# Optimization experiments

Hardware: AMD Instinct MI355X
Metric: run time of the kernel (lower is better)

Reference implementation:

```python
import jax, jax.numpy as jnp
import numpy as np

SEQ_LEN = 70      # hardcoded in original (view(-1, 70))
HIDDEN = 230
EMB = 50
VOCAB = 100000
BIG_NUM = 64
N_TOTAL = 2048
N_REL = 100       # hardcoded relation count
POS_VOCAB = 123
POS_DIM = 5
D_IN = EMB + 2 * POS_DIM


def setup_inputs() -> dict:
    key = jax.random.key(0)
    ks = jax.random.split(key, 20)
    bag = N_TOTAL // BIG_NUM
    labels = jax.random.randint(ks[3], (BIG_NUM,), 0, N_REL)
    inp = {
        "sentence": jax.random.randint(ks[0], (N_TOTAL, SEQ_LEN), 0, VOCAB),
        "pos1": jax.random.randint(ks[1], (N_TOTAL, SEQ_LEN), 0, POS_VOCAB),
        "pos2": jax.random.randint(ks[2], (N_TOTAL, SEQ_LEN), 0, POS_VOCAB),
        "total_shape": jnp.arange(BIG_NUM + 1, dtype=jnp.int32) * bag,
        "y_batch": jax.nn.one_hot(labels, N_REL, dtype=jnp.float32),
        "word_emb": jax.random.normal(ks[4], (VOCAB, EMB), jnp.float32) * 0.1,
        "pos1_table": jax.random.normal(ks[5], (POS_VOCAB, POS_DIM), jnp.float32) * 0.1,
        "pos2_table": jax.random.normal(ks[6], (POS_VOCAB, POS_DIM), jnp.float32) * 0.1,
        "W_ih_f": jax.random.normal(ks[7], (3 * HIDDEN, D_IN), jnp.float32) * 0.05,
        "W_hh_f": jax.random.normal(ks[8], (3 * HIDDEN, HIDDEN), jnp.float32) * 0.05,
        "b_ih_f": jnp.zeros((3 * HIDDEN,), jnp.float32),
        "b_hh_f": jnp.zeros((3 * HIDDEN,), jnp.float32),
        "W_ih_b": jax.random.normal(ks[9], (3 * HIDDEN, D_IN), jnp.float32) * 0.05,
        "W_hh_b": jax.random.normal(ks[10], (3 * HIDDEN, HIDDEN), jnp.float32) * 0.05,
        "b_ih_b": jnp.zeros((3 * HIDDEN,), jnp.float32),
        "b_hh_b": jnp.zeros((3 * HIDDEN,), jnp.float32),
        "attention_w": jax.random.normal(ks[11], (HIDDEN, 1), jnp.float32) * 0.1,
        "sen_a": jax.random.normal(ks[12], (HIDDEN,), jnp.float32) * 0.1,
        "sen_r": jax.random.normal(ks[13], (HIDDEN, 1), jnp.float32) * 0.1,
        "relation_embedding": jax.random.normal(ks[14], (N_REL, HIDDEN), jnp.float32) * 0.1,
        "sen_d": jax.random.normal(ks[15], (N_REL,), jnp.float32) * 0.1,
    }
    return inp


def _gru_dir(x_proj, W_hh, b_hh, reverse):
    """One GRU direction. x_proj: [N,T,3H] = x @ W_ih^T + b_ih (precomputed)."""
    N = x_proj.shape[0]
    H = W_hh.shape[1]

    def step(h, gi):
        gh = h @ W_hh.T + b_hh
        i_r, i_z, i_n = jnp.split(gi, 3, axis=-1)
        h_r, h_z, h_n = jnp.split(gh, 3, axis=-1)
        r = jax.nn.sigmoid(i_r + h_r)
        z = jax.nn.sigmoid(i_z + h_z)
        n = jnp.tanh(i_n + r * h_n)
        h = (1.0 - z) * n + z * h
        return h, h

    h0 = jnp.zeros((N, H), x_proj.dtype)
    _, ys = jax.lax.scan(step, h0, jnp.swapaxes(x_proj, 0, 1), reverse=reverse)
    return jnp.swapaxes(ys, 0, 1)  # [N,T,H]


def reference(sentence, pos1, pos2, total_shape, y_batch,
              word_emb, pos1_table, pos2_table,
              W_ih_f, W_hh_f, b_ih_f, b_hh_f,
              W_ih_b, W_hh_b, b_ih_b, b_hh_b,
              attention_w, sen_a, sen_r, relation_embedding, sen_d):
    # embedding lookup + concat -> [N, T, D_IN]
    emb = jnp.concatenate([word_emb[sentence], pos1_table[pos1], pos2_table[pos2]], axis=-1)
    gi_f = jnp.einsum('ntd,gd->ntg', emb, W_ih_f) + b_ih_f
    gi_b = jnp.einsum('ntd,gd->ntg', emb, W_ih_b) + b_ih_b
    # bidirectional GRU, then sum fwd + bwd halves (torch.add(tupf, tupb))
    tup = _gru_dir(gi_f, W_hh_f, b_hh_f, False) + _gru_dir(gi_b, W_hh_b, b_hh_b, True)  # [N,T,H]
    # word-level attention over the 70 timesteps
    word_alpha = jax.nn.softmax((jnp.tanh(tup) @ attention_w)[..., 0], axis=-1)  # [N,T]
    attention_r = jnp.einsum('nt,nth->nh', word_alpha, tup)                       # [N,H]
    repre = jnp.tanh(attention_r)
    # ragged per-bag (sentence-level) attention via segment ops
    n_total = repre.shape[0]
    seg = jnp.searchsorted(total_shape[1:], jnp.arange(n_total), side='right')   # [N] bag ids
    s = ((repre * sen_a) @ sen_r)[:, 0]                                          # [N]
    m = jax.ops.segment_max(s, seg, num_segments=BIG_NUM)
    e = jnp.exp(s - m[seg])
    denom = jax.ops.segment_sum(e, seg, num_segments=BIG_NUM)
    alpha = e / denom[seg]
    sen_s = jax.ops.segment_sum(alpha[:, None] * repre, seg, num_segments=BIG_NUM)  # [B,H]
    logits = sen_s @ relation_embedding.T + sen_d                                   # [B,100]
    prob = jax.nn.softmax(logits, axis=-1)
    # BCEWithLogitsLoss (mean over 100 classes) summed over bags
    bce = jnp.maximum(logits, 0.0) - logits * y_batch + jnp.log1p(jnp.exp(-jnp.abs(logits)))
    total_loss = jnp.sum(jnp.mean(bce, axis=-1))
    acc = (jnp.argmax(prob, axis=-1) == jnp.argmax(y_batch, axis=-1)).astype(jnp.float32)
    return total_loss, acc, prob
```

## Files before the change

### kernel.cpp

```cpp
#include <hip/hip_runtime.h>
#include <hip/hip_bf16.h>
#include <math.h>

#define SEQ 70
#define HID 230
#define G3  690
#define EMBD 50
#define DIN 60
#define NTOT 2048
#define NREL 100
#define NBAG 64
#define BAGSZ 32
#define PDIM 5
#define MB 8
#define KU 10
#define KTOT 290
#define SROWS 292


__global__ void k_zero(float* p, long n) {
    long i = (long)blockIdx.x * 256 + threadIdx.x;
    if (i < n) p[i] = 0.f;
}

__global__ void k_embed(const int* __restrict__ sent, const int* __restrict__ p1,
                        const int* __restrict__ p2,  const float* __restrict__ wemb,
                        const float* __restrict__ t1, const float* __restrict__ t2,
                        float* __restrict__ emb) {
    long idx = (long)blockIdx.x * 256 + threadIdx.x;
    long total = (long)NTOT * SEQ * DIN;
    if (idx >= total) return;
    int nt = (int)(idx / DIN);
    int j  = (int)(idx % DIN);
    float v;
    if (j < EMBD)            v = wemb[(long)sent[nt] * EMBD + j];
    else if (j < EMBD + PDIM) v = t1[p1[nt] * PDIM + (j - EMBD)];
    else                      v = t2[p2[nt] * PDIM + (j - EMBD - PDIM)];
    emb[idx] = v;
}

__global__ void k_transpose(const float* __restrict__ in, float* __restrict__ out,
                            int G, int K) {
    int idx = blockIdx.x * 256 + threadIdx.x;
    if (idx >= G * K) return;
    int g = idx / K, k = idx % K;
    out[k * G + g] = in[idx];
}


#define ROWLD(R0,R1, kk) { const float4* _p = (const float4*)s_s[kk]; \
    R0 = _p[0]; R1 = _p[1]; }

#define FMA4(WR,WZ,WN, Q, B, AR,AZ,AN) \
    AR[B+0]=fmaf(WR,Q.x,AR[B+0]); AZ[B+0]=fmaf(WZ,Q.x,AZ[B+0]); AN[B+0]=fmaf(WN,Q.x,AN[B+0]); \
    AR[B+1]=fmaf(WR,Q.y,AR[B+1]); AZ[B+1]=fmaf(WZ,Q.y,AZ[B+1]); AN[B+1]=fmaf(WN,Q.y,AN[B+1]); \
    AR[B+2]=fmaf(WR,Q.z,AR[B+2]); AZ[B+2]=fmaf(WZ,Q.z,AZ[B+2]); AN[B+2]=fmaf(WN,Q.z,AN[B+2]); \
    AR[B+3]=fmaf(WR,Q.w,AR[B+3]); AZ[B+3]=fmaf(WZ,Q.w,AZ[B+3]); AN[B+3]=fmaf(WN,Q.w,AN[B+3]);

#define FMA8(WR,WZ,WN, AR,AZ,AN, Q0,Q1) \
    FMA4(WR,WZ,WN, Q0, 0, AR,AZ,AN) FMA4(WR,WZ,WN, Q1, 4, AR,AZ,AN)

#define U2R(KB, UE, AR,AZ,AN) \
    FMA8(wR[UE],wZ[UE],wN[UE], AR,AZ,AN, ra0,ra1); \
    ROWLD(ra0,ra1, (KB)*KU+(UE)+2); \
    { int _kk = (((KB)+1)*KU + (UE)) * G3; wR[UE]=pr[_kk]; wZ[UE]=pz[_kk]; wN[UE]=pn[_kk]; } \
    FMA8(wR[UE+1],wZ[UE+1],wN[UE+1], AR,AZ,AN, rb0,rb1); \
    ROWLD(rb0,rb1, (KB)*KU+(UE)+3); \
    { int _kk = (((KB)+1)*KU + (UE)+1) * G3; wR[UE+1]=pr[_kk]; wZ[UE+1]=pz[_kk]; wN[UE+1]=pn[_kk]; }

#define U2W(KB, UE, AR,AZ,AN) \
    FMA8(wR[UE],wZ[UE],wN[UE], AR,AZ,AN, ra0,ra1); \
    ROWLD(ra0,ra1, (KB)*KU+(UE)+2); \
    { int _kk = (UE) * G3; wR[UE]=pr[_kk]; wZ[UE]=pz[_kk]; wN[UE]=pn[_kk]; } \
    FMA8(wR[UE+1],wZ[UE+1],wN[UE+1], AR,AZ,AN, rb0,rb1); \
    ROWLD(rb0,rb1, (KB)*KU+(UE)+3); \
    { int _kk = ((UE)+1) * G3; wR[UE+1]=pr[_kk]; wZ[UE+1]=pz[_kk]; wN[UE+1]=pn[_kk]; }

#define BLK10R(KB, AR,AZ,AN) \
    U2R(KB, 0, AR,AZ,AN) U2R(KB, 2, AR,AZ,AN) U2R(KB, 4, AR,AZ,AN) \
    U2R(KB, 6, AR,AZ,AN) U2R(KB, 8, AR,AZ,AN)

#define BLK10W(KB, AR,AZ,AN) \
    U2W(KB, 0, AR,AZ,AN) U2W(KB, 2, AR,AZ,AN) U2W(KB, 4, AR,AZ,AN) \
    U2W(KB, 6, AR,AZ,AN) U2W(KB, 8, AR,AZ,AN)

__global__ __launch_bounds__(256, 2) void k_gru(
    const float* __restrict__ emb,
    const float* __restrict__ wcat_f, const float* __restrict__ bih_f, const float* __restrict__ bhh_f,
    const float* __restrict__ wcat_b, const float* __restrict__ bih_b, const float* __restrict__ bhh_b,
    float* __restrict__ tup) {

    const bool rev = blockIdx.x & 1;
    const int  n0  = (blockIdx.x >> 1) * MB;
    const float* wcat = rev ? wcat_b : wcat_f;
    const float* bih  = rev ? bih_b  : bih_f;
    const float* bhh  = rev ? bhh_b  : bhh_f;
    const int tid = threadIdx.x;
    const bool act = tid < HID;

    __shared__ float s_s[SROWS][MB];

    for (int i = tid; i < SROWS * MB; i += 256) ((float*)s_s)[i] = 0.f;

    float bir = 0.f, biz = 0.f, bin_ = 0.f, bhr = 0.f, bhz = 0.f, bhn = 0.f;
    if (act) {
        bir = bih[tid]; biz = bih[HID + tid]; bin_ = bih[2 * HID + tid];
        bhr = bhh[tid]; bhz = bhh[HID + tid]; bhn = bhh[2 * HID + tid];
    }

    const float* pr = wcat + tid;
    const float* pz = wcat + HID + tid;
    const float* pn = wcat + 2 * HID + tid;

    float wR[KU], wZ[KU], wN[KU];
    if (act) {
#pragma unroll
        for (int u = 0; u < KU; ++u) {
            int kk = u * G3; wR[u] = pr[kk]; wZ[u] = pz[kk]; wN[u] = pn[kk];
        }
    }

    __syncthreads();

    for (int t = 0; t < SEQ; ++t) {
        const int tt = rev ? (SEQ - 1 - t) : t;

        for (int i = tid; i < DIN * MB; i += 256) {
            int n = i / DIN, k = i - n * DIN;
            s_s[k][n] = emb[((long)(n0 + n) * SEQ + tt) * DIN + k];
        }
        __syncthreads();

        float ar[MB], az[MB], an[MB], hr[MB], hz[MB], hn[MB];
        if (act) {
#pragma unroll
            for (int n = 0; n < MB; ++n) {
                ar[n] = bir; az[n] = biz; an[n] = bin_;
                hr[n] = bhr; hz[n] = bhz; hn[n] = bhn;
            }
            float4 ra0, ra1, rb0, rb1;
            ROWLD(ra0,ra1, 0)
            ROWLD(rb0,rb1, 1)

#pragma clang loop unroll(disable)
            for (int kb = 0; kb < 6; ++kb) { BLK10R(kb, ar,az,an) }
#pragma clang loop unroll(disable)
            for (int kb = 6; kb < 28; ++kb) { BLK10R(kb, hr,hz,hn) }
            BLK10W(28, hr,hz,hn)
        }
        __syncthreads();

        if (act) {
#pragma unroll
            for (int n = 0; n < MB; ++n) {
                float r  = 1.f / (1.f + expf(-(ar[n] + hr[n])));
                float z  = 1.f / (1.f + expf(-(az[n] + hz[n])));
                float nn = tanhf(an[n] + r * hn[n]);
                float hold = s_s[DIN + tid][n];
                float hnew = (1.f - z) * nn + z * hold;
                s_s[DIN + tid][n] = hnew;
                atomicAdd(&tup[((long)(n0 + n) * SEQ + tt) * HID + tid], hnew);
            }
        }
    }
}

__global__ __launch_bounds__(256) void k_wordattn(
    const float* __restrict__ tup, const float* __restrict__ attw,
    const float* __restrict__ sen_a, const float* __restrict__ sen_r,
    float* __restrict__ repre, float* __restrict__ sbuf) {
    const int n = blockIdx.x, tid = threadIdx.x;
    __shared__ float tl[SEQ * HID];
    __shared__ float sc[SEQ];
    __shared__ float red[4];
    for (int i = tid; i < SEQ * HID; i += 256) tl[i] = tup[(long)n * SEQ * HID + i];
    __syncthreads();
    if (tid < SEQ) {
        float s = 0.f;
        for (int h = 0; h < HID; ++h) s += tanhf(tl[tid * HID + h]) * attw[h];
        sc[tid] = s;
    }
    __syncthreads();
    if (tid == 0) {
        float m = sc[0];
        for (int t = 1; t < SEQ; ++t) m = fmaxf(m, sc[t]);
        float ssum = 0.f;
        for (int t = 0; t < SEQ; ++t) { float e = expf(sc[t] - m); sc[t] = e; ssum += e; }
        float inv = 1.f / ssum;
        for (int t = 0; t < SEQ; ++t) sc[t] *= inv;
    }
    __syncthreads();
    float part = 0.f;
    if (tid < HID) {
        float r = 0.f;
        for (int t = 0; t < SEQ; ++t) r = fmaf(sc[t], tl[t * HID + tid], r);
        float rep = tanhf(r);
        repre[(long)n * HID + tid] = rep;
        part = rep * sen_a[tid] * sen_r[tid];
    }
    for (int off = 32; off; off >>= 1) part += __shfl_down(part, off, 64);
    if ((tid & 63) == 0) red[tid >> 6] = part;
    __syncthreads();
    if (tid == 0) sbuf[n] = red[0] + red[1] + red[2] + red[3];
}

__global__ __launch_bounds__(256) void k_bag(
    const float* __restrict__ repre, const float* __restrict__ sbuf,
    const float* __restrict__ rel, const float* __restrict__ sen_d,
    const float* __restrict__ y, float* __restrict__ out, float* __restrict__ bagloss) {
    const int b = blockIdx.x, tid = threadIdx.x;
    __shared__ float al[BAGSZ];
    __shared__ float ss[HID];
    __shared__ float lg[NREL];
    if (tid == 0) {
        float m = -1e30f;
        for (int i = 0; i < BAGSZ; ++i) m = fmaxf(m, sbuf[b * BAGSZ + i]);
        float s = 0.f;
        for (int i = 0; i < BAGSZ; ++i) { float e = expf(sbuf[b * BAGSZ + i] - m); al[i] = e; s += e; }
        float inv = 1.f / s;
        for (int i = 0; i < BAGSZ; ++i) al[i] *= inv;
    }
    __syncthreads();
    if (tid < HID) {
        float acc = 0.f;
        for (int i = 0; i < BAGSZ; ++i)
            acc = fmaf(al[i], repre[(long)(b * BAGSZ + i) * HID + tid], acc);
        ss[tid] = acc;
    }
    __syncthreads();
    if (tid < NREL) {
        float acc = sen_d[tid];
        for (int h = 0; h < HID; ++h) acc = fmaf(ss[h], rel[tid * HID + h], acc);
        lg[tid] = acc;
    }
    __syncthreads();
    if (tid == 0) {
        float m = -1e30f; int am = 0;
        for (int r = 0; r < NREL; ++r) if (lg[r] > m) { m = lg[r]; am = r; }
        float s = 0.f;
        for (int r = 0; r < NREL; ++r) s += expf(lg[r] - m);
        float inv = 1.f / s;
        float ym = -1e30f; int ay = 0;
        for (int r = 0; r < NREL; ++r) { float yy = y[b * NREL + r]; if (yy > ym) { ym = yy; ay = r; } }
        out[1 + b] = (am == ay) ? 1.f : 0.f;
        float loss = 0.f;
        for (int r = 0; r < NREL; ++r) {
            float l = lg[r], yy = y[b * NREL + r];
            loss += fmaxf(l, 0.f) - l * yy + log1pf(expf(-fabsf(l)));
            out[1 + NBAG + b * NREL + r] = expf(l - m) * inv;
        }
        bagloss[b] = loss / NREL;
    }
}

__global__ void k_final(const float* __restrict__ bagloss, float* __restrict__ out) {
    if (blockIdx.x == 0 && threadIdx.x == 0) {
        float s = 0.f;
        for (int i = 0; i < NBAG; ++i) s += bagloss[i];
        out[0] = s;
    }
}

extern "C" void kernel_launch(void* const* d_in, const int* in_sizes, int n_in,
                              void* d_out, int out_size, void* d_ws, size_t ws_size,
                              hipStream_t stream) {
    const int*   sent   = (const int*)d_in[0];
    const int*   pos1   = (const int*)d_in[1];
    const int*   pos2   = (const int*)d_in[2];
    const float* ybatch = (const float*)d_in[4];
    const float* wemb   = (const float*)d_in[5];
    const float* p1tab  = (const float*)d_in[6];
    const float* p2tab  = (const float*)d_in[7];
    const float* Wih_f  = (const float*)d_in[8];
    const float* Whh_f  = (const float*)d_in[9];
    const float* bih_f  = (const float*)d_in[10];
    const float* bhh_f  = (const float*)d_in[11];
    const float* Wih_b  = (const float*)d_in[12];
    const float* Whh_b  = (const float*)d_in[13];
    const float* bih_b  = (const float*)d_in[14];
    const float* bhh_b  = (const float*)d_in[15];
    const float* attw   = (const float*)d_in[16];
    const float* sen_a  = (const float*)d_in[17];
    const float* sen_r  = (const float*)d_in[18];
    const float* rel    = (const float*)d_in[19];
    const float* sen_d  = (const float*)d_in[20];
    float* out = (float*)d_out;

    float* ws = (float*)d_ws;
    size_t off = 0;
    float* emb    = ws + off; off += (size_t)NTOT * SEQ * DIN;
    float* wcat_f = ws + off; off += (size_t)SROWS * G3;
    float* wcat_b = ws + off; off += (size_t)SROWS * G3;
    float* tup    = ws + off; off += (size_t)NTOT * SEQ * HID;
    float* repre  = ws + off; off += (size_t)NTOT * HID;
    float* sbuf   = ws + off; off += (size_t)NTOT;
    float* bagloss= ws + off; off += (size_t)NBAG;

    const long tupN = (long)NTOT * SEQ * HID;
    k_zero<<<(int)((tupN + 255) / 256), 256, 0, stream>>>(tup, tupN);

    const long embN = (long)NTOT * SEQ * DIN;
    k_embed<<<(int)((embN + 255) / 256), 256, 0, stream>>>(sent, pos1, pos2, wemb, p1tab, p2tab, emb);

    k_transpose<<<(G3 * DIN + 255) / 256, 256, 0, stream>>>(Wih_f, wcat_f, G3, DIN);
    k_transpose<<<(G3 * HID + 255) / 256, 256, 0, stream>>>(Whh_f, wcat_f + (size_t)DIN * G3, G3, HID);
    k_transpose<<<(G3 * DIN + 255) / 256, 256, 0, stream>>>(Wih_b, wcat_b, G3, DIN);
    k_transpose<<<(G3 * HID + 255) / 256, 256, 0, stream>>>(Whh_b, wcat_b + (size_t)DIN * G3, G3, HID);

    k_gru<<<(NTOT / MB) * 2, 256, 0, stream>>>(emb,
        wcat_f, bih_f, bhh_f,
        wcat_b, bih_b, bhh_b, tup);

    k_wordattn<<<NTOT, 256, 0, stream>>>(tup, attw, sen_a, sen_r, repre, sbuf);

    k_bag<<<NBAG, 256, 0, stream>>>(repre, sbuf, rel, sen_d, ybatch, out, bagloss);

    k_final<<<1, 64, 0, stream>>>(bagloss, out);
}
```

Baseline: 2.574 ms.

## Hoist GRU input projection into a separate parallel kernel before recurrence

Splits the fused GRU into a fully parallel input-projection kernel (x@W_ih + b_ih over all timesteps) writing a large gi buffer, and a recurrent kernel that only does the 230-wide h@W_hh product per step. The aim is to take about a fifth of the FMAs off the sequential critical path and run them with much more parallelism. In exchange it writes and reads back a large fp32 intermediate of about 2*2048*70*690 floats. The old fused kernel is kept as a fallback when the workspace is too small.

After: 2.514 ms. 1.02x faster.

```diff
diff --git a/kernel.cpp b/kernel.cpp
--- a/kernel.cpp
+++ b/kernel.cpp
@@ -15,7 +15,10 @@
 #define MB 8
 #define KU 10
 #define KTOT 290
-#define SROWS 292
+#define SROWS_F 292
+#define SROWS_H 232
+#define WROWS_H 240
+#define TCH 10
 
 
 __global__ void k_zero(float* p, long n) {
@@ -47,6 +50,13 @@
     out[k * G + g] = in[idx];
 }
 
+__global__ void k_dupeh(float* __restrict__ w) {
+    int idx = blockIdx.x * 256 + threadIdx.x;
+    if (idx >= 10 * G3) return;
+    int i = idx / G3, g = idx % G3;
+    w[(HID + i) * G3 + g] = w[i * G3 + g];
+}
+
 
 #define ROWLD(R0,R1, kk) { const float4* _p = (const float4*)s_s[kk]; \
     R0 = _p[0]; R1 = _p[1]; }
@@ -84,7 +94,128 @@
     U2W(KB, 0, AR,AZ,AN) U2W(KB, 2, AR,AZ,AN) U2W(KB, 4, AR,AZ,AN) \
     U2W(KB, 6, AR,AZ,AN) U2W(KB, 8, AR,AZ,AN)
 
-__global__ __launch_bounds__(256, 2) void k_gru(
+__global__ __launch_bounds__(256, 2) void k_gi(
+    const float* __restrict__ emb,
+    const float* __restrict__ wih_f, const float* __restrict__ bih_f,
+    const float* __restrict__ wih_b, const float* __restrict__ bih_b,
+    float* __restrict__ gi) {
+    const int bid = blockIdx.x;
+    const int dir = bid & 1;
+    const int r   = bid >> 1;
+    const int tc  = r % (SEQ / TCH);
+    const int n0  = (r / (SEQ / TCH)) * MB;
+    const float* wih = dir ? wih_b : wih_f;
+    const float* bih = dir ? bih_b : bih_f;
+    const int tid = threadIdx.x;
+    const bool act = tid < HID;
+
+    __shared__ float e_s[DIN][MB];
+
+    float bir = 0.f, biz = 0.f, bin_ = 0.f;
+    if (act) { bir = bih[tid]; biz = bih[HID + tid]; bin_ = bih[2 * HID + tid]; }
+    const float* pw = wih + tid;
+
+    for (int tt = tc * TCH; tt < tc * TCH + TCH; ++tt) {
+        for (int i = tid; i < DIN * MB; i += 256) {
+            int n = i / DIN, k = i - n * DIN;
+            e_s[k][n] = emb[((long)(n0 + n) * SEQ + tt) * DIN + k];
+        }
+        __syncthreads();
+        if (act) {
+            float ar[MB], az[MB], an[MB];
+#pragma unroll
+            for (int n = 0; n < MB; ++n) { ar[n] = bir; az[n] = biz; an[n] = bin_; }
+            for (int k = 0; k < DIN; ++k) {
+                float wr = pw[k * G3], wz = pw[k * G3 + HID], wn = pw[k * G3 + 2 * HID];
+                float4 e0 = *(const float4*)&e_s[k][0];
+                float4 e1 = *(const float4*)&e_s[k][4];
+                FMA8(wr, wz, wn, ar, az, an, e0, e1)
+            }
+#pragma unroll
+            for (int n = 0; n < MB; ++n) {
+                long gb = ((long)(dir ? NTOT : 0) + (n0 + n)) * ((long)SEQ * G3) + (long)tt * G3;
+                gi[gb + tid] = ar[n];
+                gi[gb + HID + tid] = az[n];
+                gi[gb + 2 * HID + tid] = an[n];
+            }
+        }
+        __syncthreads();
+    }
+}
+
+__global__ __launch_bounds__(256, 2) void k_gru2(
+    const float* __restrict__ gi,
+    const float* __restrict__ whh_f, const float* __restrict__ bhh_f,
+    const float* __restrict__ whh_b, const float* __restrict__ bhh_b,
+    float* __restrict__ tup) {
+
+    const bool rev = blockIdx.x & 1;
+    const int  n0  = (blockIdx.x >> 1) * MB;
+    const float* whh = rev ? whh_b : whh_f;
+    const float* bhh = rev ? bhh_b : bhh_f;
+    const int tid = threadIdx.x;
+    const bool act = tid < HID;
+
+    __shared__ float s_s[SROWS_H][MB];
+
+    for (int i = tid; i < SROWS_H * MB; i += 256) ((float*)s_s)[i] = 0.f;
+
+    float bhr = 0.f, bhz = 0.f, bhn = 0.f;
+    if (act) { bhr = bhh[tid]; bhz = bhh[HID + tid]; bhn = bhh[2 * HID + tid]; }
+
+    const float* pr = whh + tid;
+    const float* pz = whh + HID + tid;
+    const float* pn = whh + 2 * HID + tid;
+
+    float wR[KU], wZ[KU], wN[KU];
+    if (act) {
+#pragma unroll
+        for (int u = 0; u < KU; ++u) {
+            int kk = u * G3; wR[u] = pr[kk]; wZ[u] = pz[kk]; wN[u] = pn[kk];
+        }
+    }
+
+    __syncthreads();
+
+    for (int t = 0; t < SEQ; ++t) {
+        const int tt = rev ? (SEQ - 1 - t) : t;
+
+        float ar[MB], az[MB], an[MB], hr[MB], hz[MB], hn[MB];
+        if (act) {
+#pragma unroll
+            for (int n = 0; n < MB; ++n) {
+                long gb = ((long)(rev ? NTOT : 0) + (n0 + n)) * ((long)SEQ * G3) + (long)tt * G3;
+                ar[n] = gi[gb + tid];
+                az[n] = gi[gb + HID + tid];
+                an[n] = gi[gb + 2 * HID + tid];
+                hr[n] = bhr; hz[n] = bhz; hn[n] = bhn;
+            }
+            float4 ra0, ra1, rb0, rb1;
+            ROWLD(ra0, ra1, 0)
+            ROWLD(rb0, rb1, 1)
+
+#pragma clang loop unroll(disable)
+            for (int kb = 0; kb < 23; ++kb) { BLK10R(kb, hr, hz, hn) }
+        }
+        __syncthreads();
+
+        if (act) {
+#pragma unroll
+            for (int n = 0; n < MB; ++n) {
+                float r  = 1.f / (1.f + expf(-(ar[n] + hr[n])));
+                float z  = 1.f / (1.f + expf(-(az[n] + hz[n])));
+                float nn = tanhf(an[n] + r * hn[n]);
+                float hold = s_s[tid][n];
+                float hnew = (1.f - z) * nn + z * hold;
+                s_s[tid][n] = hnew;
+                atomicAdd(&tup[((long)(n0 + n) * SEQ + tt) * HID + tid], hnew);
+            }
+        }
+        __syncthreads();
+    }
+}
+
+__global__ __launch_bounds__(256, 2) void k_gruF(
     const float* __restrict__ emb,
     const float* __restrict__ wcat_f, const float* __restrict__ bih_f, const float* __restrict__ bhh_f,
     const float* __restrict__ wcat_b, const float* __restrict__ bih_b, const float* __restrict__ bhh_b,
@@ -98,9 +229,9 @@
     const int tid = threadIdx.x;
     const bool act = tid < HID;
 
-    __shared__ float s_s[SROWS][MB];
-
-    for (int i = tid; i < SROWS * MB; i += 256) ((float*)s_s)[i] = 0.f;
+    __shared__ float s_s[SROWS_F][MB];
+
+    for (int i = tid; i < SROWS_F * MB; i += 256) ((float*)s_s)[i] = 0.f;
 
     float bir = 0.f, biz = 0.f, bin_ = 0.f, bhr = 0.f, bhz = 0.f, bhn = 0.f;
     if (act) {
@@ -139,14 +270,14 @@
                 hr[n] = bhr; hz[n] = bhz; hn[n] = bhn;
             }
             float4 ra0, ra1, rb0, rb1;
-            ROWLD(ra0,ra1, 0)
-            ROWLD(rb0,rb1, 1)
+            ROWLD(ra0, ra1, 0)
+            ROWLD(rb0, rb1, 1)
 
 #pragma clang loop unroll(disable)
-            for (int kb = 0; kb < 6; ++kb) { BLK10R(kb, ar,az,an) }
+            for (int kb = 0; kb < 6; ++kb) { BLK10R(kb, ar, az, an) }
 #pragma clang loop unroll(disable)
-            for (int kb = 6; kb < 28; ++kb) { BLK10R(kb, hr,hz,hn) }
-            BLK10W(28, hr,hz,hn)
+            for (int kb = 6; kb < 28; ++kb) { BLK10R(kb, hr, hz, hn) }
+            BLK10W(28, hr, hz, hn)
         }
         __syncthreads();
 
@@ -289,12 +420,20 @@
     float* ws = (float*)d_ws;
     size_t off = 0;
     float* emb    = ws + off; off += (size_t)NTOT * SEQ * DIN;
-    float* wcat_f = ws + off; off += (size_t)SROWS * G3;
-    float* wcat_b = ws + off; off += (size_t)SROWS * G3;
+    float* wcat_f = ws + off; off += (size_t)SROWS_F * G3;
+    float* wcat_b = ws + off; off += (size_t)SROWS_F * G3;
+    float* wih_f  = ws + off; off += (size_t)DIN * G3;
+    float* wih_b  = ws + off; off += (size_t)DIN * G3;
+    float* whh_f  = ws + off; off += (size_t)WROWS_H * G3;
+    float* whh_b  = ws + off; off += (size_t)WROWS_H * G3;
     float* tup    = ws + off; off += (size_t)NTOT * SEQ * HID;
     float* repre  = ws + off; off += (size_t)NTOT * HID;
     float* sbuf   = ws + off; off += (size_t)NTOT;
     float* bagloss= ws + off; off += (size_t)NBAG;
+    float* gi     = ws + off; off += (size_t)2 * NTOT * SEQ * G3;
+    const size_t need_split = off;
+
+    const bool split = (ws_size / sizeof(float)) >= need_split;
 
     const long tupN = (long)NTOT * SEQ * HID;
     k_zero<<<(int)((tupN + 255) / 256), 256, 0, stream>>>(tup, tupN);
@@ -302,14 +441,28 @@
     const long embN = (long)NTOT * SEQ * DIN;
     k_embed<<<(int)((embN + 255) / 256), 256, 0, stream>>>(sent, pos1, pos2, wemb, p1tab, p2tab, emb);
 
-    k_transpose<<<(G3 * DIN + 255) / 256, 256, 0, stream>>>(Wih_f, wcat_f, G3, DIN);
-    k_transpose<<<(G3 * HID + 255) / 256, 256, 0, stream>>>(Whh_f, wcat_f + (size_t)DIN * G3, G3, HID);
-    k_transpose<<<(G3 * DIN + 255) / 256, 256, 0, stream>>>(Wih_b, wcat_b, G3, DIN);
-    k_transpose<<<(G3 * HID + 255) / 256, 256, 0, stream>>>(Whh_b, wcat_b + (size_t)DIN * G3, G3, HID);
-
-    k_gru<<<(NTOT / MB) * 2, 256, 0, stream>>>(emb,
-        wcat_f, bih_f, bhh_f,
-        wcat_b, bih_b, bhh_b, tup);
+    if (split) {
+        k_transpose<<<(G3 * DIN + 255) / 256, 256, 0, stream>>>(Wih_f, wih_f, G3, DIN);
+        k_transpose<<<(G3 * DIN + 255) / 256, 256, 0, stream>>>(Wih_b, wih_b, G3, DIN);
+        k_transpose<<<(G3 * HID + 255) / 256, 256, 0, stream>>>(Whh_f, whh_f, G3, HID);
+        k_transpose<<<(G3 * HID + 255) / 256, 256, 0, stream>>>(Whh_b, whh_b, G3, HID);
+        k_dupeh<<<(10 * G3 + 255) / 256, 256, 0, stream>>>(whh_f);
+        k_dupeh<<<(10 * G3 + 255) / 256, 256, 0, stream>>>(whh_b);
+
+        k_gi<<<(NTOT / MB) * (SEQ / TCH) * 2, 256, 0, stream>>>(
+            emb, wih_f, bih_f, wih_b, bih_b, gi);
+        k_gru2<<<(NTOT / MB) * 2, 256, 0, stream>>>(
+            gi, whh_f, bhh_f, whh_b, bhh_b, tup);
+    } else {
+        k_transpose<<<(G3 * DIN + 255) / 256, 256, 0, stream>>>(Wih_f, wcat_f, G3, DIN);
+        k_transpose<<<(G3 * HID + 255) / 256, 256, 0, stream>>>(Whh_f, wcat_f + (size_t)DIN * G3, G3, HID);
+        k_transpose<<<(G3 * DIN + 255) / 256, 256, 0, stream>>>(Wih_b, wcat_b, G3, DIN);
+        k_transpose<<<(G3 * HID + 255) / 256, 256, 0, stream>>>(Whh_b, wcat_b + (size_t)DIN * G3, G3, HID);
+
+        k_gruF<<<(NTOT / MB) * 2, 256, 0, stream>>>(emb,
+            wcat_f, bih_f, bhh_f,
+            wcat_b, bih_b, bhh_b, tup);
+    }
 
     k_wordattn<<<NTOT, 256, 0, stream>>>(tup, attw, sen_a, sen_r, repre, sbuf);
 
```
